# Optimization experiments

Measured on AMD Instinct MI355X. Metric: run time of the kernel, lower is better.

## Reference

```python
import jax, jax.numpy as jnp
import numpy as np

# irreps structure: 256x0e + 128x1e + 64x2e (same for all three layers)
MULS = [256, 128, 64]
DIMS = [1, 3, 5]  # 2l+1 for l=0,1,2


def _split(x):
    """Split flat feature [N, 960] into per-irrep blocks [N, mul, 2l+1]."""
    blocks, o = [], 0
    for m, d in zip(MULS, DIMS):
        blocks.append(x[:, o:o + m * d].reshape(-1, m, d))
        o += m * d
    return blocks


def _merge(blocks):
    n = blocks[0].shape[0]
    return jnp.concatenate([b.reshape(n, -1) for b in blocks], axis=1)


def _irrep_linear(blocks, ws):
    # o3.Linear between identical irreps: per-l matmul over the multiplicity
    # axis, path_normalization='element' (single path) -> scale 1/sqrt(mul_in).
    return [jnp.einsum('nui,uw->nwi', b, w) / np.sqrt(b.shape[1])
            for b, w in zip(blocks, ws)]


def _norm_act(blocks):
    # e3nn NormActivation(gelu), normalize=True: x * gelu(||x||) / ||x||
    out = []
    for b in blocks:
        n = jnp.sqrt(jnp.sum(b * b, axis=-1, keepdims=True))  # [N, mul, 1]
        safe_n = jnp.where(n > 0, n, 1.0)
        out.append(b * (jax.nn.gelu(n, approximate=False) / safe_n))
    return out


def setup_inputs() -> dict:
    key = jax.random.key(0)
    ks = jax.random.split(key, 7)
    N = 65536
    D = sum(m * d for m, d in zip(MULS, DIMS))  # 960
    inp = {'x': jax.random.normal(ks[0], (N, D), dtype=jnp.float32)}
    names = ['W0_0', 'W0_1', 'W0_2', 'W1_0', 'W1_1', 'W1_2']
    shapes = [(256, 256), (128, 128), (64, 64)] * 2
    for k, name, s in zip(ks[1:], names, shapes):
        inp[name] = jax.random.normal(k, s, dtype=jnp.float32)
    return inp


def reference(x, W0_0, W0_1, W0_2, W1_0, W1_1, W1_2):
    blocks = _split(x)
    blocks = _irrep_linear(blocks, [W0_0, W0_1, W0_2])
    blocks = _norm_act(blocks)
    blocks = _irrep_linear(blocks, [W1_0, W1_1, W1_2])
    return _merge(blocks)
```

## Files before the change

kernel.cpp:

```cpp
#include <hip/hip_runtime.h>


typedef __bf16 v8bf  __attribute__((ext_vector_type(8)));
typedef __bf16 v2bf  __attribute__((ext_vector_type(2)));
typedef float  v4f   __attribute__((ext_vector_type(4)));

__device__ __forceinline__ unsigned short bfbits(float x) {
    __bf16 h = (__bf16)x;
    return __builtin_bit_cast(unsigned short, h);
}

__device__ __forceinline__ float phi_from_n(float n) {
    float z = n * 0.70710678118654752f;
    float t = __builtin_amdgcn_rcpf(fmaf(0.3275911f, z, 1.0f));
    float p = t * fmaf(t, fmaf(t, fmaf(t, fmaf(t, 1.061405429f, -1.453152027f),
                                       1.421413741f), -0.284496736f), 0.254829592f);
    float e = __builtin_amdgcn_exp2f(z * z * -1.4426950408889634f);
    return fmaf(p * e, -0.5f, 1.0f);
}

__global__ __launch_bounds__(256) void wt_prep(
    const float* __restrict__ w0, const float* __restrict__ w1,
    const float* __restrict__ w2, const float* __restrict__ w3,
    const float* __restrict__ w4, const float* __restrict__ w5,
    unsigned short* __restrict__ out)
{
    int t = blockIdx.x * 256 + threadIdx.x;
    if (t >= 172032) return;
    int s = (t < 65536) ? 0 : (t < 81920) ? 1 : (t < 86016) ? 2
          : (t < 151552) ? 3 : (t < 167936) ? 4 : 5;
    int base = (s == 0) ? 0 : (s == 1) ? 65536 : (s == 2) ? 81920
             : (s == 3) ? 86016 : (s == 4) ? 151552 : 167936;
    int lg   = (s == 0 || s == 3) ? 8 : (s == 1 || s == 4) ? 7 : 6;
    float scl = (s == 0 || s == 3) ? 0.0625f
              : (s == 1 || s == 4) ? 0.08838834764831845f : 0.125f;
    const float* p = (s == 0) ? w0 : (s == 1) ? w1 : (s == 2) ? w2
                   : (s == 3) ? w3 : (s == 4) ? w4 : w5;
    int loc = t - base;
    int w = loc >> lg;
    int u = loc & ((1 << lg) - 1);
    out[t] = bfbits(p[(u << lg) + w] * scl);
}

template<int U, int D, int OFF, int ROWS>
__device__ __forceinline__ void irrep_block(
    const float* __restrict__ x,
    const unsigned short* __restrict__ wt0,
    const unsigned short* __restrict__ wt1,
    float* __restrict__ out,
    unsigned short* __restrict__ lds,
    int tile)
{
    constexpr int MT   = (ROWS * D) / 16;
    constexpr int NPW  = U / 64;
    constexpr int KT   = U / 32;
    constexpr int NR16 = ROWS / 16;
    static_assert(ROWS * D * U <= 32768, "LDS overflow");

    const int tid  = threadIdx.x;
    const int lane = tid & 63;
    const int wid  = tid >> 6;
    const int row0 = tile * ROWS;
    const int wcol = lane & 15;
    const int kcol = (lane >> 4) << 3;
    const int g4   = (lane >> 4) << 2;

    if constexpr (D == 1) {
        #pragma unroll
        for (int o = 0; o < (ROWS * (U / 8)) / 256; ++o) {
            int oct = o * 256 + tid;
            int row = oct / (U / 8);
            int u0  = (oct % (U / 8)) * 8;
            const float4* p =
                reinterpret_cast<const float4*>(x + (long)(row0 + row) * 960 + OFF + u0);
            float4 fa = p[0], fb = p[1];
            v8bf hv = { (__bf16)fa.x, (__bf16)fa.y, (__bf16)fa.z, (__bf16)fa.w,
                        (__bf16)fb.x, (__bf16)fb.y, (__bf16)fb.z, (__bf16)fb.w };
            int idx = (row * U + u0) ^ ((row & 7) << 3);
            *reinterpret_cast<v8bf*>(&lds[idx]) = hv;
        }
    } else {
        constexpr int PAIRS = U / 2;
        #pragma unroll
        for (int g = 0; g < (ROWS * PAIRS) / 256; ++g) {
            int gid = g * 256 + tid;
            int row = gid / PAIRS;
            int u0  = (gid % PAIRS) * 2;
            const float2* p = reinterpret_cast<const float2*>(
                x + (long)(row0 + row) * 960 + OFF + u0 * D);
            float f[2 * D];
            #pragma unroll
            for (int j = 0; j < D; ++j) { float2 q = p[j]; f[2*j] = q.x; f[2*j+1] = q.y; }
            #pragma unroll
            for (int i = 0; i < D; ++i) {
                int R = i * ROWS + row;
                int idx = (R * U + u0) ^ ((R & 7) << 3);
                v2bf h2 = { (__bf16)f[i], (__bf16)f[D + i] };
                *reinterpret_cast<v2bf*>(&lds[idx]) = h2;
            }
        }
    }

    v4f acc[MT][NPW];
    v8bf bpre[NPW];

    auto issueB = [&](const unsigned short* __restrict__ wt, int kt) {
        #pragma unroll
        for (int nt = 0; nt < NPW; ++nt) {
            int w = (wid * NPW + nt) * 16 + wcol;
            bpre[nt] = *reinterpret_cast<const v8bf*>(wt + w * U + kt * 32 + kcol);
        }
    };

    auto run_layer = [&](const unsigned short* __restrict__ wt) {
        #pragma unroll
        for (int mt = 0; mt < MT; ++mt)
            #pragma unroll
            for (int nt = 0; nt < NPW; ++nt) {
                v4f z = {0.f, 0.f, 0.f, 0.f};
                acc[mt][nt] = z;
            }
        #pragma unroll
        for (int kt = 0; kt < KT; ++kt) {
            v8bf bcur[NPW];
            #pragma unroll
            for (int nt = 0; nt < NPW; ++nt) bcur[nt] = bpre[nt];
            if (kt + 1 < KT) issueB(wt, kt + 1);
            #pragma unroll
            for (int mt = 0; mt < MT; ++mt) {
                int R = mt * 16 + wcol;
                int idx = (R * U + kt * 32 + kcol) ^ ((R & 7) << 3);
                v8bf a = *reinterpret_cast<const v8bf*>(&lds[idx]);
                #pragma unroll
                for (int nt = 0; nt < NPW; ++nt)
                    acc[mt][nt] = __builtin_amdgcn_mfma_f32_16x16x32_bf16(
                        a, bcur[nt], acc[mt][nt], 0, 0, 0);
            }
        }
    };

    issueB(wt0, 0);
    __syncthreads();

    run_layer(wt0);
    __syncthreads();

    issueB(wt1, 0);

    #pragma unroll
    for (int nt = 0; nt < NPW; ++nt) {
        int w = (wid * NPW + nt) * 16 + wcol;
        #pragma unroll
        for (int h = 0; h < NR16; ++h) {
            #pragma unroll
            for (int r = 0; r < 4; ++r) {
                float n;
                if constexpr (D == 1) {
                    n = __builtin_fabsf(acc[h][nt][r]);
                } else {
                    float s = 0.f;
                    #pragma unroll
                    for (int i = 0; i < D; ++i) {
                        float v = acc[i * NR16 + h][nt][r];
                        s += v * v;
                    }
                    n = __builtin_amdgcn_sqrtf(s);
                }
                float fac = phi_from_n(n);
                int nr = h * 16 + g4 + r;
                #pragma unroll
                for (int i = 0; i < D; ++i) {
                    int R = i * ROWS + nr;
                    int idx = (R * U + w) ^ ((R & 7) << 3);
                    lds[idx] = bfbits(acc[i * NR16 + h][nt][r] * fac);
                }
            }
        }
    }
    __syncthreads();

    run_layer(wt1);

    #pragma unroll
    for (int nt = 0; nt < NPW; ++nt) {
        int w = (wid * NPW + nt) * 16 + wcol;
        #pragma unroll
        for (int h = 0; h < NR16; ++h) {
            #pragma unroll
            for (int r = 0; r < 4; ++r) {
                int n = row0 + h * 16 + g4 + r;
                float* po = out + (long)n * 960 + OFF + w * D;
                #pragma unroll
                for (int i = 0; i < D; ++i)
                    po[i] = acc[i * NR16 + h][nt][r];
            }
        }
    }
}

__global__ __launch_bounds__(256, 2) void fused_all(
    const float* __restrict__ x,
    const unsigned short* __restrict__ ws,
    float* __restrict__ out)
{
    __shared__ unsigned short lds[32768];
    int bid = blockIdx.x;
    if (bid < 512)
        irrep_block<256, 1,   0, 128>(x, ws + 0,     ws + 86016,  out, lds, bid);
    else if (bid < 1536)
        irrep_block<128, 3, 256,  64>(x, ws + 65536, ws + 151552, out, lds, bid - 512);
    else
        irrep_block< 64, 5, 640,  64>(x, ws + 81920, ws + 167936, out, lds, bid - 1536);
}

extern "C" void kernel_launch(void* const* d_in, const int* in_sizes, int n_in,
                              void* d_out, int out_size, void* d_ws, size_t ws_size,
                              hipStream_t stream)
{
    const float* x  = (const float*)d_in[0];
    const float* W0 = (const float*)d_in[1];
    const float* W1 = (const float*)d_in[2];
    const float* W2 = (const float*)d_in[3];
    const float* W3 = (const float*)d_in[4];
    const float* W4 = (const float*)d_in[5];
    const float* W5 = (const float*)d_in[6];
    unsigned short* ws = (unsigned short*)d_ws;
    float* out = (float*)d_out;

    wt_prep<<<672, 256, 0, stream>>>(W0, W1, W2, W3, W4, W5, ws);
    fused_all<<<2560, 256, 0, stream>>>(x, ws, out);
}
```

Before: 135.4 us.

## Use 512-thread blocks with per-irrep wave tiling over columns and rows

Doubles the block size to eight waves and adds template parameters that split each irrep's GEMM across waves by output-column groups and, for the l=2 block, row groups. Each wave holds fewer accumulators, and more waves per CU are available to hide global-load and MFMA latency. The cost is more redundant LDS reads of the A fragments across waves, plus a tighter register budget under the new launch bounds.

```diff
diff --git a/kernel.cpp b/kernel.cpp
--- a/kernel.cpp
+++ b/kernel.cpp
@@ -42,7 +42,7 @@
     out[t] = bfbits(p[(u << lg) + w] * scl);
 }
 
-template<int U, int D, int OFF, int ROWS>
+template<int U, int D, int OFF, int ROWS, int WN, int WM>
 __device__ __forceinline__ void irrep_block(
     const float* __restrict__ x,
     const unsigned short* __restrict__ wt0,
@@ -51,15 +51,19 @@
     unsigned short* __restrict__ lds,
     int tile)
 {
-    constexpr int MT   = (ROWS * D) / 16;
-    constexpr int NPW  = U / 64;
+    constexpr int THR  = 512;
+    constexpr int NR16 = ROWS / 16;
+    constexpr int NRH  = NR16 / WM;
+    constexpr int NPW  = U / (WN * 16);
     constexpr int KT   = U / 32;
-    constexpr int NR16 = ROWS / 16;
     static_assert(ROWS * D * U <= 32768, "LDS overflow");
+    static_assert(WN * WM == 8, "8 waves");
 
     const int tid  = threadIdx.x;
     const int lane = tid & 63;
     const int wid  = tid >> 6;
+    const int wn   = wid % WN;
+    const int hg   = wid / WN;
     const int row0 = tile * ROWS;
     const int wcol = lane & 15;
     const int kcol = (lane >> 4) << 3;
@@ -67,8 +71,8 @@
 
     if constexpr (D == 1) {
         #pragma unroll
-        for (int o = 0; o < (ROWS * (U / 8)) / 256; ++o) {
-            int oct = o * 256 + tid;
+        for (int o = 0; o < (ROWS * (U / 8)) / THR; ++o) {
+            int oct = o * THR + tid;
             int row = oct / (U / 8);
             int u0  = (oct % (U / 8)) * 8;
             const float4* p =
@@ -82,8 +86,8 @@
     } else {
         constexpr int PAIRS = U / 2;
         #pragma unroll
-        for (int g = 0; g < (ROWS * PAIRS) / 256; ++g) {
-            int gid = g * 256 + tid;
+        for (int g = 0; g < (ROWS * PAIRS) / THR; ++g) {
+            int gid = g * THR + tid;
             int row = gid / PAIRS;
             int u0  = (gid % PAIRS) * 2;
             const float2* p = reinterpret_cast<const float2*>(
@@ -101,25 +105,27 @@
         }
     }
 
-    v4f acc[MT][NPW];
+    v4f acc[D][NRH][NPW];
     v8bf bpre[NPW];
 
     auto issueB = [&](const unsigned short* __restrict__ wt, int kt) {
         #pragma unroll
         for (int nt = 0; nt < NPW; ++nt) {
-            int w = (wid * NPW + nt) * 16 + wcol;
+            int w = (wn * NPW + nt) * 16 + wcol;
             bpre[nt] = *reinterpret_cast<const v8bf*>(wt + w * U + kt * 32 + kcol);
         }
     };
 
     auto run_layer = [&](const unsigned short* __restrict__ wt) {
         #pragma unroll
-        for (int mt = 0; mt < MT; ++mt)
-            #pragma unroll
-            for (int nt = 0; nt < NPW; ++nt) {
-                v4f z = {0.f, 0.f, 0.f, 0.f};
-                acc[mt][nt] = z;
-            }
+        for (int i = 0; i < D; ++i)
+            #pragma unroll
+            for (int hh = 0; hh < NRH; ++hh)
+                #pragma unroll
+                for (int nt = 0; nt < NPW; ++nt) {
+                    v4f z = {0.f, 0.f, 0.f, 0.f};
+                    acc[i][hh][nt] = z;
+                }
         #pragma unroll
         for (int kt = 0; kt < KT; ++kt) {
             v8bf bcur[NPW];
@@ -127,14 +133,17 @@
             for (int nt = 0; nt < NPW; ++nt) bcur[nt] = bpre[nt];
             if (kt + 1 < KT) issueB(wt, kt + 1);
             #pragma unroll
-            for (int mt = 0; mt < MT; ++mt) {
-                int R = mt * 16 + wcol;
-                int idx = (R * U + kt * 32 + kcol) ^ ((R & 7) << 3);
-                v8bf a = *reinterpret_cast<const v8bf*>(&lds[idx]);
-                #pragma unroll
-                for (int nt = 0; nt < NPW; ++nt)
-                    acc[mt][nt] = __builtin_amdgcn_mfma_f32_16x16x32_bf16(
-                        a, bcur[nt], acc[mt][nt], 0, 0, 0);
+            for (int i = 0; i < D; ++i) {
+                #pragma unroll
+                for (int hh = 0; hh < NRH; ++hh) {
+                    int R = i * ROWS + (hg * NRH + hh) * 16 + wcol;
+                    int idx = (R * U + kt * 32 + kcol) ^ ((R & 7) << 3);
+                    v8bf a = *reinterpret_cast<const v8bf*>(&lds[idx]);
+                    #pragma unroll
+                    for (int nt = 0; nt < NPW; ++nt)
+                        acc[i][hh][nt] = __builtin_amdgcn_mfma_f32_16x16x32_bf16(
+                            a, bcur[nt], acc[i][hh][nt], 0, 0, 0);
+                }
             }
         }
     };
@@ -149,30 +158,30 @@
 
     #pragma unroll
     for (int nt = 0; nt < NPW; ++nt) {
-        int w = (wid * NPW + nt) * 16 + wcol;
-        #pragma unroll
-        for (int h = 0; h < NR16; ++h) {
+        int w = (wn * NPW + nt) * 16 + wcol;
+        #pragma unroll
+        for (int hh = 0; hh < NRH; ++hh) {
             #pragma unroll
             for (int r = 0; r < 4; ++r) {
                 float n;
                 if constexpr (D == 1) {
-                    n = __builtin_fabsf(acc[h][nt][r]);
+                    n = __builtin_fabsf(acc[0][hh][nt][r]);
                 } else {
                     float s = 0.f;
                     #pragma unroll
                     for (int i = 0; i < D; ++i) {
-                        float v = acc[i * NR16 + h][nt][r];
+                        float v = acc[i][hh][nt][r];
                         s += v * v;
                     }
                     n = __builtin_amdgcn_sqrtf(s);
                 }
                 float fac = phi_from_n(n);
-                int nr = h * 16 + g4 + r;
+                int nr = (hg * NRH + hh) * 16 + g4 + r;
                 #pragma unroll
                 for (int i = 0; i < D; ++i) {
                     int R = i * ROWS + nr;
                     int idx = (R * U + w) ^ ((R & 7) << 3);
-                    lds[idx] = bfbits(acc[i * NR16 + h][nt][r] * fac);
+                    lds[idx] = bfbits(acc[i][hh][nt][r] * fac);
                 }
             }
         }
@@ -183,22 +192,22 @@
 
     #pragma unroll
     for (int nt = 0; nt < NPW; ++nt) {
-        int w = (wid * NPW + nt) * 16 + wcol;
-        #pragma unroll
-        for (int h = 0; h < NR16; ++h) {
+        int w = (wn * NPW + nt) * 16 + wcol;
+        #pragma unroll
+        for (int hh = 0; hh < NRH; ++hh) {
             #pragma unroll
             for (int r = 0; r < 4; ++r) {
-                int n = row0 + h * 16 + g4 + r;
+                int n = row0 + (hg * NRH + hh) * 16 + g4 + r;
                 float* po = out + (long)n * 960 + OFF + w * D;
                 #pragma unroll
                 for (int i = 0; i < D; ++i)
-                    po[i] = acc[i * NR16 + h][nt][r];
+                    po[i] = acc[i][hh][nt][r];
             }
         }
     }
 }
 
-__global__ __launch_bounds__(256, 2) void fused_all(
+__global__ __launch_bounds__(512, 4) void fused_all(
     const float* __restrict__ x,
     const unsigned short* __restrict__ ws,
     float* __restrict__ out)
@@ -206,11 +215,11 @@
     __shared__ unsigned short lds[32768];
     int bid = blockIdx.x;
     if (bid < 512)
-        irrep_block<256, 1,   0, 128>(x, ws + 0,     ws + 86016,  out, lds, bid);
+        irrep_block<256, 1,   0, 128, 8, 1>(x, ws + 0,     ws + 86016,  out, lds, bid);
     else if (bid < 1536)
-        irrep_block<128, 3, 256,  64>(x, ws + 65536, ws + 151552, out, lds, bid - 512);
+        irrep_block<128, 3, 256,  64, 8, 1>(x, ws + 65536, ws + 151552, out, lds, bid - 512);
     else
-        irrep_block< 64, 5, 640,  64>(x, ws + 81920, ws + 167936, out, lds, bid - 1536);
+        irrep_block< 64, 5, 640,  64, 4, 2>(x, ws + 81920, ws + 167936, out, lds, bid - 1536);
 }
 
 extern "C" void kernel_launch(void* const* d_in, const int* in_sizes, int n_in,
@@ -228,5 +237,5 @@
     float* out = (float*)d_out;
 
     wt_prep<<<672, 256, 0, stream>>>(W0, W1, W2, W3, W4, W5, ws);
-    fused_all<<<2560, 256, 0, stream>>>(x, ws, out);
-}
+    fused_all<<<2560, 512, 0, stream>>>(x, ws, out);
+}
```

After: 146.9 us. +8.5%, slower.
